# Performance work log

Hardware: AMD Instinct MI355X
Metric: run time of the kernel (lower is better)

## Reference

```python
import jax, jax.numpy as jnp
import numpy as np

N_NODES = 50000
N_EDGES = 800000
NUM_GRAPHS = 256
BN_EPS = 1e-5


def setup_inputs() -> dict:
    key = jax.random.key(0)
    ks = jax.random.split(key, 16)
    in_dim, hid, out_dim = 64, 128, 1
    s = lambda k, shape, fan: jax.random.normal(k, shape, jnp.float32) / np.sqrt(fan)
    inp = {
        'x': jax.random.normal(ks[0], (N_NODES, in_dim), jnp.float32),
        'edge_index': jax.random.randint(ks[1], (2, N_EDGES), 0, N_NODES, jnp.int64),
        'batch': jnp.sort(jax.random.randint(ks[2], (N_NODES,), 0, NUM_GRAPHS, jnp.int64)),
        # SAGEConv layer 0 (in_dim->hid): Wn aggregated-neighbor weight (with bias), Wr root weight
        'Wn0': s(ks[3], (in_dim, hid), in_dim), 'Wr0': s(ks[4], (in_dim, hid), in_dim), 'b0': jnp.zeros((hid,), jnp.float32),
        'Wn1': s(ks[5], (hid, hid), hid), 'Wr1': s(ks[6], (hid, hid), hid), 'b1': jnp.zeros((hid,), jnp.float32),
        'Wn2': s(ks[7], (hid, hid), hid), 'Wr2': s(ks[8], (hid, hid), hid), 'b2': jnp.zeros((hid,), jnp.float32),
        'gamma': jnp.ones((3, hid), jnp.float32), 'beta': jnp.zeros((3, hid), jnp.float32),
        'fc1_W': s(ks[9], (hid, hid // 2), hid), 'fc1_b': jnp.zeros((hid // 2,), jnp.float32),
        'fc2_W': s(ks[10], (hid // 2, out_dim), hid // 2), 'fc2_b': jnp.zeros((out_dim,), jnp.float32),
    }
    return inp


def _sage_mean(x, src, dst, inv_deg, Wn, Wr, b):
    # mean-aggregate neighbor features then linear: lin_l(mean_j x_j) + lin_r(x_i)
    agg = jax.ops.segment_sum(x[src], dst, num_segments=N_NODES) * inv_deg
    return agg @ Wn + x @ Wr + b


def _bn_relu(h, g, bta):
    mu = jnp.mean(h, axis=0)
    var = jnp.var(h, axis=0)
    return jax.nn.relu((h - mu) * jax.lax.rsqrt(var + BN_EPS) * g + bta)


def reference(x, edge_index, batch, Wn0, Wr0, b0, Wn1, Wr1, b1, Wn2, Wr2, b2,
              gamma, beta, fc1_W, fc1_b, fc2_W, fc2_b):
    src, dst = edge_index[0], edge_index[1]
    deg = jax.ops.segment_sum(jnp.ones((src.shape[0],), x.dtype), dst, num_segments=N_NODES)
    inv_deg = (1.0 / jnp.maximum(deg, 1.0))[:, None]  # [N,1]

    h = _bn_relu(_sage_mean(x, src, dst, inv_deg, Wn0, Wr0, b0), gamma[0], beta[0])
    h = _bn_relu(_sage_mean(h, src, dst, inv_deg, Wn1, Wr1, b1), gamma[1], beta[1])
    h = _bn_relu(_sage_mean(h, src, dst, inv_deg, Wn2, Wr2, b2), gamma[2], beta[2])

    # global mean pool over graphs
    pooled = jax.ops.segment_sum(h, batch, num_segments=NUM_GRAPHS)
    cnt = jax.ops.segment_sum(jnp.ones((h.shape[0],), h.dtype), batch, num_segments=NUM_GRAPHS)
    pooled = pooled / jnp.maximum(cnt, 1.0)[:, None]

    z = jax.nn.relu(pooled @ fc1_W + fc1_b)
    return jax.nn.sigmoid(z @ fc2_W + fc2_b)  # [NUM_GRAPHS, 1]
```

## Files before the change

### kernel.cpp

```cpp
#include <hip/hip_runtime.h>

#define N_NODES 50000
#define N_EDGES 800000
#define NUM_GRAPHS 256
#define HID 128
#define IN_DIM 64
#define BN_EPS 1e-5f
#define SPREAD 16
#define NB 196
#define BUCKET 256
#define SCHUNK 4096
#define NCHUNK 196
#define PX_BLKS 1563
#define W0_BLKS 8
#define W1_BLKS 16
#define GB_BLKS 196

typedef __attribute__((ext_vector_type(8))) short bf16x8;
typedef __attribute__((ext_vector_type(4))) float f32x4;

__device__ __forceinline__ float bf2f(unsigned short u){ union{unsigned i;float f;}c; c.i=((unsigned)u)<<16; return c.f; }
__device__ __forceinline__ float bflo(unsigned w){ union{unsigned i;float f;}c; c.i=w<<16; return c.f; }
__device__ __forceinline__ float bfhi(unsigned w){ union{unsigned i;float f;}c; c.i=w&0xFFFF0000u; return c.f; }
__device__ __forceinline__ unsigned short f2bf(float f){ union{float f;unsigned i;}c; c.f=f; unsigned r=c.i+0x7FFF+((c.i>>16)&1); return (unsigned short)(r>>16); }
__device__ __forceinline__ unsigned fpack(float a, float b){
  union{float f;unsigned i;}ca,cb; ca.f=a; cb.f=b;
  unsigned ra=((ca.i+0x7FFF+((ca.i>>16)&1))>>16)&0xFFFFu;
  unsigned rb=(cb.i+0x7FFF+((cb.i>>16)&1))&0xFFFF0000u;
  return ra|rb;
}
__device__ __forceinline__ void acc8(float* a, uint4 u){
  a[0]+=bflo(u.x); a[1]+=bfhi(u.x); a[2]+=bflo(u.y); a[3]+=bfhi(u.y);
  a[4]+=bflo(u.z); a[5]+=bfhi(u.z); a[6]+=bflo(u.w); a[7]+=bfhi(u.w);
}

__global__ __launch_bounds__(256) void k_hist(const int* __restrict__ dst, int* __restrict__ bcount){
  __shared__ int h[NB];
  int t = threadIdx.x;
  for(int i=t;i<NB;i+=256) h[i]=0;
  __syncthreads();
  int base = blockIdx.x*SCHUNK;
  int n = min(SCHUNK, N_EDGES-base);
  for(int v=t; v<n; v+=256) atomicAdd(&h[dst[base+v]>>8], 1);
  __syncthreads();
  for(int i=t;i<NB;i+=256) if(h[i]) atomicAdd(&bcount[i], h[i]);
}

__global__ __launch_bounds__(256) void k_scatter_pack(const int* __restrict__ src, const int* __restrict__ dst,
      const int* __restrict__ bcount, int* __restrict__ bfill, unsigned* __restrict__ pairs,
      const float* __restrict__ x, unsigned short* __restrict__ H0,
      const float* __restrict__ Wn0, const float* __restrict__ Wr0, unsigned short* __restrict__ Bp0,
      const float* __restrict__ Wn1, const float* __restrict__ Wr1, unsigned short* __restrict__ Bp1,
      const float* __restrict__ Wn2, const float* __restrict__ Wr2, unsigned short* __restrict__ Bp2,
      const int* __restrict__ batch, int* __restrict__ gstart){
  __shared__ int h[NB], lbase[NB], gbase[NB], cur[NB];
  __shared__ int sc[256];
  __shared__ unsigned staged[SCHUNK];
  int blk = blockIdx.x, t = threadIdx.x;
  if(blk < NCHUNK){
    for(int i=t;i<NB;i+=256) h[i]=0;
    __syncthreads();
    int base = blk*SCHUNK;
    int n = min(SCHUNK, N_EDGES-base);
    for(int v=t; v<n; v+=256) atomicAdd(&h[dst[base+v]>>8], 1);
    __syncthreads();
    int bc = (t<NB)? bcount[t] : 0;
    sc[t]=bc; __syncthreads();
    for(int off=1;off<256;off<<=1){ int u=(t>=off)?sc[t-off]:0; __syncthreads(); sc[t]+=u; __syncthreads(); }
    int bb_t = sc[t]-bc;
    __syncthreads();
    int hv = (t<NB)? h[t] : 0;
    sc[t]=hv; __syncthreads();
    for(int off=1;off<256;off<<=1){ int u=(t>=off)?sc[t-off]:0; __syncthreads(); sc[t]+=u; __syncthreads(); }
    if(t<NB){ lbase[t]=sc[t]-hv; cur[t]=0; if(hv) gbase[t] = bb_t + atomicAdd(&bfill[t], hv); }
    __syncthreads();
    for(int v=t; v<n; v+=256){
      int s = src[base+v], d = dst[base+v];
      int b = d>>8;
      int rr = atomicAdd(&cur[b], 1);
      staged[lbase[b]+rr] = (unsigned)s | ((unsigned)(d&255)<<16) | ((unsigned)b<<24);
    }
    __syncthreads();
    for(int i=t; i<n; i+=256){
      unsigned p = staged[i];
      int b = (int)(p>>24);
      pairs[gbase[b] + (i - lbase[b])] = p;
    }
  } else if(blk < NCHUNK+PX_BLKS){
    int tid = (blk-NCHUNK)*256 + t;
    if(tid < N_NODES*8){
      int row = tid>>3, q = tid&7;
      float4 a = ((const float4*)x)[(size_t)row*16 + q*2];
      float4 b = ((const float4*)x)[(size_t)row*16 + q*2 + 1];
      uint4 o;
      o.x = fpack(a.x,a.y); o.y = fpack(a.z,a.w);
      o.z = fpack(b.x,b.y); o.w = fpack(b.z,b.w);
      ((uint4*)H0)[(size_t)row*8 + q] = o;
    }
  } else if(blk < NCHUNK+PX_BLKS+W0_BLKS+2*W1_BLKS){
    const float *Wn, *Wr; unsigned short* Bp; int KH, base;
    if(blk < NCHUNK+PX_BLKS+W0_BLKS){ Wn=Wn0; Wr=Wr0; Bp=Bp0; KH=IN_DIM; base=NCHUNK+PX_BLKS; }
    else if(blk < NCHUNK+PX_BLKS+W0_BLKS+W1_BLKS){ Wn=Wn1; Wr=Wr1; Bp=Bp1; KH=HID; base=NCHUNK+PX_BLKS+W0_BLKS; }
    else { Wn=Wn2; Wr=Wr2; Bp=Bp2; KH=HID; base=NCHUNK+PX_BLKS+W0_BLKS+W1_BLKS; }
    int NKS = (2*KH)/32;
    int id = (blk-base)*256 + t;
    if(id < 8*NKS*64){
      int lane = id & 63;
      int ks = (id>>6) % NKS;
      int nt = (id>>6) / NKS;
      int quad = lane>>4, m = lane&15;
      int c = nt*16 + m;
      unsigned short v[8];
      #pragma unroll
      for(int j=0;j<8;j++){
        int k = ks*32 + quad*8 + j;
        float w = (k < KH) ? Wn[(size_t)k*HID + c] : Wr[(size_t)(k-KH)*HID + c];
        v[j] = f2bf(w);
      }
      uint4 o;
      o.x = ((unsigned)v[1]<<16)|v[0]; o.y = ((unsigned)v[3]<<16)|v[2];
      o.z = ((unsigned)v[5]<<16)|v[4]; o.w = ((unsigned)v[7]<<16)|v[6];
      ((uint4*)Bp)[id] = o;
    }
  } else {
    int id = (blk - (NCHUNK+PX_BLKS+W0_BLKS+2*W1_BLKS))*256 + t;
    if(id < N_NODES){
      int b = batch[id];
      if(id == 0){
        for(int g=0; g<=b; g++) gstart[g] = 0;
      } else {
        int pv = batch[id-1];
        if(pv != b) for(int g=pv+1; g<=b; g++) gstart[g] = id;
      }
      if(id == N_NODES-1){
        for(int g=b+1; g<=NUM_GRAPHS; g++) gstart[g] = N_NODES;
      }
    }
  }
}

__global__ __launch_bounds__(1024) void k_csr(const unsigned* __restrict__ pairs, const int* __restrict__ bcount,
                int* __restrict__ rowptr, float* __restrict__ invdeg, unsigned short* __restrict__ eidx){
  __shared__ int cnt[BUCKET], cur[BUCKET], sc[BUCKET];
  __shared__ int bb[2];
  int t = threadIdx.x;
  int b = blockIdx.x;
  if(t==0){ bb[0]=0; bb[1]=0; }
  if(t<BUCKET) cnt[t]=0;
  __syncthreads();
  if(t<NB){
    int c = bcount[t];
    if(t<b)  atomicAdd(&bb[0], c);
    if(t<=b) atomicAdd(&bb[1], c);
  }
  __syncthreads();
  int e0 = bb[0], e1 = bb[1];
  int node0 = b*BUCKET;
  for(int i=e0+t; i<e1; i+=1024) atomicAdd(&cnt[(int)((pairs[i]>>16)&0xFF)], 1);
  __syncthreads();
  if(t<BUCKET) sc[t]=cnt[t];
  __syncthreads();
  for(int off=1;off<BUCKET;off<<=1){
    int u=0;
    if(t<BUCKET && t>=off) u=sc[t-off];
    __syncthreads();
    if(t<BUCKET) sc[t]+=u;
    __syncthreads();
  }
  if(t<BUCKET && node0+t < N_NODES){
    int pre = sc[t]-cnt[t] + e0;
    rowptr[node0+t] = pre;
    cur[t] = pre;
    invdeg[node0+t] = 1.0f/(float)max(cnt[t],1);
  }
  if(b==0 && t==0) rowptr[N_NODES] = N_EDGES;
  __syncthreads();
  for(int i=e0+t; i<e1; i+=1024){
    unsigned p = pairs[i];
    int pos = atomicAdd(&cur[(p>>16)&0xFF], 1);
    eidx[pos] = (unsigned short)(p & 0xFFFF);
  }
}

template<int KH>
__global__ __launch_bounds__(256) void k_agg_gemm(const unsigned short* __restrict__ H,
                     const unsigned short* __restrict__ eidx, const int* __restrict__ rowptr,
                     const float* __restrict__ invdeg,
                     const unsigned short* __restrict__ Bp, const float* __restrict__ bias,
                     unsigned short* __restrict__ raw,
                     float* __restrict__ psum, float* __restrict__ psq){
  const int NKS = (2*KH)/32;
  const int LKS = KH/32;
  const int F8  = KH/8;
  const int RPI = 64/F8;
  const int LDA = KH + 4;
  __shared__ unsigned short Alds[16*LDA];
  int wave = threadIdx.x>>6, lane = threadIdx.x&63;
  int row0b = blockIdx.x*16;

  int r = lane / F8, q = lane % F8;
  #pragma unroll
  for(int j=0; j<4; j++){
    int li = wave*4 + j;
    int n = row0b + li;
    int b = rowptr[n], e = rowptr[n+1];
    float acc[8] = {0,0,0,0,0,0,0,0};
    int i = b + r;
    for(; i + 3*RPI < e; i += 4*RPI){
      int s0 = eidx[i], s1 = eidx[i+RPI], s2 = eidx[i+2*RPI], s3 = eidx[i+3*RPI];
      uint4 u0 = *(const uint4*)(H + (size_t)s0*KH + q*8);
      uint4 u1 = *(const uint4*)(H + (size_t)s1*KH + q*8);
      uint4 u2 = *(const uint4*)(H + (size_t)s2*KH + q*8);
      uint4 u3 = *(const uint4*)(H + (size_t)s3*KH + q*8);
      acc8(acc,u0); acc8(acc,u1); acc8(acc,u2); acc8(acc,u3);
    }
    for(; i + RPI < e; i += 2*RPI){
      int s0 = eidx[i], s1 = eidx[i+RPI];
      uint4 u0 = *(const uint4*)(H + (size_t)s0*KH + q*8);
      uint4 u1 = *(const uint4*)(H + (size_t)s1*KH + q*8);
      acc8(acc,u0); acc8(acc,u1);
    }
    for(; i < e; i += RPI){
      int s0 = eidx[i];
      uint4 u0 = *(const uint4*)(H + (size_t)s0*KH + q*8);
      acc8(acc,u0);
    }
    #pragma unroll
    for(int off = F8; off < 64; off <<= 1){
      #pragma unroll
      for(int k=0;k<8;k++) acc[k] += __shfl_xor(acc[k], off, 64);
    }
    if(lane < F8){
      float id = invdeg[n];
      uint4 o;
      o.x = fpack(acc[0]*id, acc[1]*id); o.y = fpack(acc[2]*id, acc[3]*id);
      o.z = fpack(acc[4]*id, acc[5]*id); o.w = fpack(acc[6]*id, acc[7]*id);
      *(uint4*)(Alds + li*LDA + lane*8) = o;
    }
  }
  __syncthreads();

  int m = lane&15, quad = lane>>4;
  const unsigned short* Arow = Alds + m*LDA + quad*8;
  const unsigned short* Hrow = H + (size_t)(row0b+m)*KH + quad*8;
  f32x4 facc[2];
  facc[0] = (f32x4){0.f,0.f,0.f,0.f};
  facc[1] = (f32x4){0.f,0.f,0.f,0.f};
  #pragma unroll 1
  for(int ks=0; ks<NKS; ks++){
    bf16x8 a = (ks < LKS) ? *(const bf16x8*)(Arow + ks*32)
                          : *(const bf16x8*)(Hrow + (size_t)(ks-LKS)*32);
    const unsigned short* bp = Bp + (((size_t)(wave*2)*NKS + ks)*64 + lane)*8;
    bf16x8 b0 = *(const bf16x8*)(bp);
    bf16x8 b1 = *(const bf16x8*)(bp + (size_t)NKS*64*8);
    facc[0] = __builtin_amdgcn_mfma_f32_16x16x32_bf16(a, b0, facc[0], 0, 0, 0);
    facc[1] = __builtin_amdgcn_mfma_f32_16x16x32_bf16(a, b1, facc[1], 0, 0, 0);
  }
  int sp = blockIdx.x & (SPREAD-1);
  #pragma unroll
  for(int nt=0;nt<2;nt++){
    int col = wave*32 + nt*16 + m;
    float bv = bias[col];
    float s = 0.f, s2 = 0.f;
    #pragma unroll
    for(int reg=0;reg<4;reg++){
      float v = facc[nt][reg] + bv;
      int row = row0b + quad*4 + reg;
      raw[(size_t)row*HID + col] = f2bf(v);
      s += v; s2 += v*v;
    }
    s  += __shfl_xor(s, 16, 64);  s  += __shfl_xor(s, 32, 64);
    s2 += __shfl_xor(s2, 16, 64); s2 += __shfl_xor(s2, 32, 64);
    if(quad==0){
      atomicAdd(&psum[sp*HID+col], s);
      atomicAdd(&psq [sp*HID+col], s2);
    }
  }
}

__global__ __launch_bounds__(256) void k_transform(const unsigned short* __restrict__ raw,
      const float* __restrict__ psum, const float* __restrict__ psq,
      const float* __restrict__ gamma, const float* __restrict__ beta,
      unsigned short* __restrict__ Hout){
  __shared__ float s_sc[HID], s_sf[HID];
  int t = threadIdx.x;
  if(t < HID){
    float s=0.f, s2=0.f;
    #pragma unroll
    for(int i=0;i<SPREAD;i++){ s += psum[i*HID+t]; s2 += psq[i*HID+t]; }
    float mu  = s  * (1.0f/(float)N_NODES);
    float var = s2 * (1.0f/(float)N_NODES) - mu*mu;
    float rstd = rsqrtf(var + BN_EPS);
    float sc = rstd * gamma[t];
    s_sc[t] = sc; s_sf[t] = beta[t] - mu*sc;
  }
  __syncthreads();
  int tid = blockIdx.x*256 + t;
  if(tid >= N_NODES*16) return;
  int q = tid & 15;
  uint4 u = ((const uint4*)raw)[tid];
  float f0 = fmaxf(fmaf(bflo(u.x), s_sc[q*8+0], s_sf[q*8+0]), 0.f);
  float f1 = fmaxf(fmaf(bfhi(u.x), s_sc[q*8+1], s_sf[q*8+1]), 0.f);
  float f2 = fmaxf(fmaf(bflo(u.y), s_sc[q*8+2], s_sf[q*8+2]), 0.f);
  float f3 = fmaxf(fmaf(bfhi(u.y), s_sc[q*8+3], s_sf[q*8+3]), 0.f);
  float f4 = fmaxf(fmaf(bflo(u.z), s_sc[q*8+4], s_sf[q*8+4]), 0.f);
  float f5 = fmaxf(fmaf(bfhi(u.z), s_sc[q*8+5], s_sf[q*8+5]), 0.f);
  float f6 = fmaxf(fmaf(bflo(u.w), s_sc[q*8+6], s_sf[q*8+6]), 0.f);
  float f7 = fmaxf(fmaf(bfhi(u.w), s_sc[q*8+7], s_sf[q*8+7]), 0.f);
  uint4 o;
  o.x = fpack(f0,f1); o.y = fpack(f2,f3); o.z = fpack(f4,f5); o.w = fpack(f6,f7);
  ((uint4*)Hout)[tid] = o;
}

__global__ __launch_bounds__(256) void k_poolmlp(const unsigned short* __restrict__ raw,
      const int* __restrict__ gstart,
      const float* __restrict__ psum, const float* __restrict__ psq,
      const float* __restrict__ gamma, const float* __restrict__ beta,
      const float* __restrict__ fc1W, const float* __restrict__ fc1b,
      const float* __restrict__ fc2W, const float* __restrict__ fc2b,
      float* __restrict__ out){
  __shared__ float s_sc[HID], s_sf[HID];
  __shared__ float red[16][HID];
  __shared__ float p[HID];
  int g = blockIdx.x, t = threadIdx.x;
  if(t < HID){
    float s=0.f, s2=0.f;
    #pragma unroll
    for(int i=0;i<SPREAD;i++){ s += psum[i*HID+t]; s2 += psq[i*HID+t]; }
    float mu  = s  * (1.0f/(float)N_NODES);
    float var = s2 * (1.0f/(float)N_NODES) - mu*mu;
    float rstd = rsqrtf(var + BN_EPS);
    float sc = rstd * gamma[t];
    s_sc[t] = sc; s_sf[t] = beta[t] - mu*sc;
  }
  __syncthreads();
  int r0 = gstart[g], r1 = gstart[g+1];
  int q = t & 15, rr = t >> 4;
  float acc[8] = {0,0,0,0,0,0,0,0};
  for(int n = r0 + rr; n < r1; n += 16){
    uint4 u = ((const uint4*)raw)[(size_t)n*16 + q];
    acc[0] += fmaxf(fmaf(bflo(u.x), s_sc[q*8+0], s_sf[q*8+0]), 0.f);
    acc[1] += fmaxf(fmaf(bfhi(u.x), s_sc[q*8+1], s_sf[q*8+1]), 0.f);
    acc[2] += fmaxf(fmaf(bflo(u.y), s_sc[q*8+2], s_sf[q*8+2]), 0.f);
    acc[3] += fmaxf(fmaf(bfhi(u.y), s_sc[q*8+3], s_sf[q*8+3]), 0.f);
    acc[4] += fmaxf(fmaf(bflo(u.z), s_sc[q*8+4], s_sf[q*8+4]), 0.f);
    acc[5] += fmaxf(fmaf(bfhi(u.z), s_sc[q*8+5], s_sf[q*8+5]), 0.f);
    acc[6] += fmaxf(fmaf(bflo(u.w), s_sc[q*8+6], s_sf[q*8+6]), 0.f);
    acc[7] += fmaxf(fmaf(bfhi(u.w), s_sc[q*8+7], s_sf[q*8+7]), 0.f);
  }
  #pragma unroll
  for(int k=0;k<8;k++) red[rr][q*8+k] = acc[k];
  __syncthreads();
  if(t < HID){
    float s = 0.f;
    #pragma unroll
    for(int j=0;j<16;j++) s += red[j][t];
    float ic = 1.0f / fmaxf((float)(r1 - r0), 1.0f);
    p[t] = s * ic;
  }
  __syncthreads();
  if(t < 64){
    float z = fc1b[t];
    #pragma unroll 4
    for(int k=0;k<HID;k++) z += p[k]*fc1W[k*64 + t];
    z = fmaxf(z, 0.f);
    float v = z * fc2W[t];
    #pragma unroll
    for(int off=32; off>0; off>>=1) v += __shfl_down(v, off, 64);
    if(t==0) out[g] = 1.0f/(1.0f + expf(-(v + fc2b[0])));
  }
}

extern "C" void kernel_launch(void* const* d_in, const int* in_sizes, int n_in,
                              void* d_out, int out_size, void* d_ws, size_t ws_size,
                              hipStream_t stream){
  const float* x    = (const float*)d_in[0];
  const int*   ei   = (const int*)d_in[1];
  const int*   batch= (const int*)d_in[2];
  const float* Wn0=(const float*)d_in[3]; const float* Wr0=(const float*)d_in[4]; const float* b0=(const float*)d_in[5];
  const float* Wn1=(const float*)d_in[6]; const float* Wr1=(const float*)d_in[7]; const float* b1=(const float*)d_in[8];
  const float* Wn2=(const float*)d_in[9]; const float* Wr2=(const float*)d_in[10]; const float* b2=(const float*)d_in[11];
  const float* gamma=(const float*)d_in[12]; const float* beta=(const float*)d_in[13];
  const float* fc1W=(const float*)d_in[14]; const float* fc1b=(const float*)d_in[15];
  const float* fc2W=(const float*)d_in[16]; const float* fc2b=(const float*)d_in[17];
  float* out = (float*)d_out;

  char* ws = (char*)d_ws;
  size_t off = 0;
  auto alloc = [&](size_t bytes)->char*{ char* p = ws + off; off += (bytes + 255) & ~(size_t)255; return p; };

  char* zero0   = ws + off;
  int*   bcount = (int*)alloc((size_t)NB*4);
  int*   bfill  = (int*)alloc((size_t)NB*4);
  float* pstats = (float*)alloc((size_t)3*2*SPREAD*HID*4);
  size_t zbytes = (size_t)((ws + off) - zero0);

  unsigned short* H0  = (unsigned short*)alloc((size_t)N_NODES*IN_DIM*2);
  unsigned short* H1  = (unsigned short*)alloc((size_t)N_NODES*HID*2);
  unsigned short* H2  = (unsigned short*)alloc((size_t)N_NODES*HID*2);
  unsigned short* raw = (unsigned short*)alloc((size_t)N_NODES*HID*2);
  unsigned short* Bp0 = (unsigned short*)alloc((size_t)8*4*64*8*2);
  unsigned short* Bp1 = (unsigned short*)alloc((size_t)8*8*64*8*2);
  unsigned short* Bp2 = (unsigned short*)alloc((size_t)8*8*64*8*2);
  float* invdeg = (float*)alloc((size_t)N_NODES*4);
  int* rowptr   = (int*)alloc((size_t)(N_NODES+1)*4);
  unsigned short* eidx = (unsigned short*)alloc((size_t)N_EDGES*2);
  unsigned* pairs = (unsigned*)alloc((size_t)N_EDGES*4);
  int* gstart   = (int*)alloc((size_t)(NUM_GRAPHS+1)*4);

  auto psumL = [&](int l){ return pstats + (size_t)l*2*SPREAD*HID; };
  auto psqL  = [&](int l){ return pstats + (size_t)l*2*SPREAD*HID + (size_t)SPREAD*HID; };

  const int* src = ei;
  const int* dst = ei + N_EDGES;

  hipMemsetAsync(zero0, 0, zbytes, stream);

  k_hist<<<NCHUNK, 256, 0, stream>>>(dst, bcount);
  k_scatter_pack<<<NCHUNK+PX_BLKS+W0_BLKS+2*W1_BLKS+GB_BLKS, 256, 0, stream>>>(src, dst, bcount, bfill, pairs,
      x, H0, Wn0, Wr0, Bp0, Wn1, Wr1, Bp1, Wn2, Wr2, Bp2, batch, gstart);
  k_csr<<<NB, 1024, 0, stream>>>(pairs, bcount, rowptr, invdeg, eidx);

  const int AG_BLKS = (N_NODES + 15)/16;

  k_agg_gemm<IN_DIM><<<AG_BLKS, 256, 0, stream>>>(H0, eidx, rowptr, invdeg, Bp0, b0, raw, psumL(0), psqL(0));
  k_transform<<<(N_NODES*16)/256, 256, 0, stream>>>(raw, psumL(0), psqL(0), gamma+0*HID, beta+0*HID, H1);
  k_agg_gemm<HID><<<AG_BLKS, 256, 0, stream>>>(H1, eidx, rowptr, invdeg, Bp1, b1, raw, psumL(1), psqL(1));
  k_transform<<<(N_NODES*16)/256, 256, 0, stream>>>(raw, psumL(1), psqL(1), gamma+1*HID, beta+1*HID, H2);
  k_agg_gemm<HID><<<AG_BLKS, 256, 0, stream>>>(H2, eidx, rowptr, invdeg, Bp2, b2, raw, psumL(2), psqL(2));

  k_poolmlp<<<NUM_GRAPHS, 256, 0, stream>>>(raw, gstart, psumL(2), psqL(2), gamma+2*HID, beta+2*HID,
      fc1W, fc1b, fc2W, fc2b, out);
}
```

Before: 278.9 us.

## Restructure neighbor gather: one row per 16 lanes, stage edge indices in LDS

The aggregation phase now gives each quarter-wave its own destination row and processes all four rows of a wave at once, instead of looping over four rows with the whole wave per row. The block's edge index slice is first staged into shared memory when it fits in 512 entries, and the gather loop is unrolled to eight outstanding loads. This aims to raise memory-level parallelism and cut the cross-lane shuffle reductions. In exchange it adds extra barriers and an LDS staging pass, and load balance suffers when row degrees within a wave vary widely.

```diff
diff --git a/kernel.cpp b/kernel.cpp
--- a/kernel.cpp
+++ b/kernel.cpp
@@ -192,51 +192,69 @@
   const int NKS = (2*KH)/32;
   const int LKS = KH/32;
   const int F8  = KH/8;
-  const int RPI = 64/F8;
+  const int SPL = 16/F8;
   const int LDA = KH + 4;
+  const int EDGE_CAP = 512;
   __shared__ unsigned short Alds[16*LDA];
-  int wave = threadIdx.x>>6, lane = threadIdx.x&63;
+  __shared__ unsigned short Elds[EDGE_CAP];
+  __shared__ int rp[17];
+  int t = threadIdx.x;
+  int wave = t>>6, lane = t&63;
   int row0b = blockIdx.x*16;
 
-  int r = lane / F8, q = lane % F8;
-  #pragma unroll
-  for(int j=0; j<4; j++){
-    int li = wave*4 + j;
-    int n = row0b + li;
-    int b = rowptr[n], e = rowptr[n+1];
-    float acc[8] = {0,0,0,0,0,0,0,0};
-    int i = b + r;
-    for(; i + 3*RPI < e; i += 4*RPI){
-      int s0 = eidx[i], s1 = eidx[i+RPI], s2 = eidx[i+2*RPI], s3 = eidx[i+3*RPI];
-      uint4 u0 = *(const uint4*)(H + (size_t)s0*KH + q*8);
-      uint4 u1 = *(const uint4*)(H + (size_t)s1*KH + q*8);
-      uint4 u2 = *(const uint4*)(H + (size_t)s2*KH + q*8);
-      uint4 u3 = *(const uint4*)(H + (size_t)s3*KH + q*8);
-      acc8(acc,u0); acc8(acc,u1); acc8(acc,u2); acc8(acc,u3);
-    }
-    for(; i + RPI < e; i += 2*RPI){
-      int s0 = eidx[i], s1 = eidx[i+RPI];
-      uint4 u0 = *(const uint4*)(H + (size_t)s0*KH + q*8);
-      uint4 u1 = *(const uint4*)(H + (size_t)s1*KH + q*8);
-      acc8(acc,u0); acc8(acc,u1);
-    }
-    for(; i < e; i += RPI){
-      int s0 = eidx[i];
-      uint4 u0 = *(const uint4*)(H + (size_t)s0*KH + q*8);
-      acc8(acc,u0);
-    }
-    #pragma unroll
-    for(int off = F8; off < 64; off <<= 1){
-      #pragma unroll
-      for(int k=0;k<8;k++) acc[k] += __shfl_xor(acc[k], off, 64);
-    }
-    if(lane < F8){
-      float id = invdeg[n];
-      uint4 o;
-      o.x = fpack(acc[0]*id, acc[1]*id); o.y = fpack(acc[2]*id, acc[3]*id);
-      o.z = fpack(acc[4]*id, acc[5]*id); o.w = fpack(acc[6]*id, acc[7]*id);
-      *(uint4*)(Alds + li*LDA + lane*8) = o;
-    }
+  if(t < 17) rp[t] = rowptr[row0b + t];
+  __syncthreads();
+  int ebase = rp[0];
+  int etot  = rp[16] - ebase;
+  bool fits = (etot <= EDGE_CAP);
+  if(fits){
+    for(int i=t; i<etot; i+=256) Elds[i] = eidx[ebase + i];
+  }
+  __syncthreads();
+
+  int rr = lane >> 4;
+  int h  = (SPL==1) ? 0 : ((lane>>3)&1);
+  int q  = lane & (F8-1);
+  int li = wave*4 + rr;
+  int b = rp[li] - ebase, e = rp[li+1] - ebase;
+  float acc[8] = {0,0,0,0,0,0,0,0};
+
+#define LDH(s) (*(const uint4*)(H + (size_t)(s)*KH + q*8))
+#define GBODY(FETCH) { \
+    int i = b + h; \
+    for(; i + 7*SPL < e; i += 8*SPL){ \
+      int s0=FETCH(i), s1=FETCH(i+SPL), s2=FETCH(i+2*SPL), s3=FETCH(i+3*SPL), \
+          s4=FETCH(i+4*SPL), s5=FETCH(i+5*SPL), s6=FETCH(i+6*SPL), s7=FETCH(i+7*SPL); \
+      uint4 u0=LDH(s0),u1=LDH(s1),u2=LDH(s2),u3=LDH(s3),u4=LDH(s4),u5=LDH(s5),u6=LDH(s6),u7=LDH(s7); \
+      acc8(acc,u0); acc8(acc,u1); acc8(acc,u2); acc8(acc,u3); \
+      acc8(acc,u4); acc8(acc,u5); acc8(acc,u6); acc8(acc,u7); \
+    } \
+    for(; i + 3*SPL < e; i += 4*SPL){ \
+      int s0=FETCH(i), s1=FETCH(i+SPL), s2=FETCH(i+2*SPL), s3=FETCH(i+3*SPL); \
+      uint4 u0=LDH(s0),u1=LDH(s1),u2=LDH(s2),u3=LDH(s3); \
+      acc8(acc,u0); acc8(acc,u1); acc8(acc,u2); acc8(acc,u3); \
+    } \
+    for(; i < e; i += SPL){ \
+      int s0=FETCH(i); uint4 u0=LDH(s0); acc8(acc,u0); \
+    } }
+#define FL(i) ((int)Elds[(i)])
+#define FG(i) ((int)eidx[ebase + (i)])
+  if(fits){ GBODY(FL) } else { GBODY(FG) }
+#undef FL
+#undef FG
+#undef GBODY
+#undef LDH
+
+  if(SPL==2){
+    #pragma unroll
+    for(int k=0;k<8;k++) acc[k] += __shfl_xor(acc[k], 8, 64);
+  }
+  if(h==0){
+    float id = invdeg[row0b + li];
+    uint4 o;
+    o.x = fpack(acc[0]*id, acc[1]*id); o.y = fpack(acc[2]*id, acc[3]*id);
+    o.z = fpack(acc[4]*id, acc[5]*id); o.w = fpack(acc[6]*id, acc[7]*id);
+    *(uint4*)(Alds + li*LDA + q*8) = o;
   }
   __syncthreads();
 
```

Result: faster. 264.0 us (median of 2 runs) (-5.4%).
